# Performance work log

Hardware: AMD Instinct MI355X
Metric: run time of the kernel (lower is better)

The kernel has to match this reference:

```python
import jax, jax.numpy as jnp
import numpy as np

N, E, A, S = 100000, 1600000, 500000, 50000
F_IN, W, LAYERS = 64, 64, 3


def setup_inputs() -> dict:
    key = jax.random.key(0)
    ks = jax.random.split(key, 20)

    def glorot(k, shape):
        fan_in = shape[-2]
        return jax.random.normal(k, shape, dtype=jnp.float32) / jnp.sqrt(jnp.float32(fan_in))

    return {
        "x": jax.random.normal(ks[0], (N, F_IN), dtype=jnp.float32),
        "edge_src": jax.random.randint(ks[1], (E,), 0, N, dtype=jnp.int32),
        "edge_dst": jax.random.randint(ks[2], (E,), 0, N, dtype=jnp.int32),
        "gather_idx": jax.random.randint(ks[3], (A,), 0, N, dtype=jnp.int32),
        "seg_idx": jax.random.randint(ks[4], (A,), 0, S, dtype=jnp.int32),
        # GraphConv 0: lin_root (no bias) + lin_rel (bias)
        "w_root0": glorot(ks[5], (F_IN, W)),
        "w_rel0": glorot(ks[6], (F_IN, W)),
        "b0": jnp.zeros((W,), jnp.float32),
        # hidden GraphConv layers, stacked
        "w_root_h": glorot(ks[7], (LAYERS - 1, W, W)),
        "w_rel_h": glorot(ks[8], (LAYERS - 1, W, W)),
        "b_h": jnp.zeros((LAYERS - 1, W), jnp.float32),
        # MLP head
        "fc1_w": glorot(ks[9], (W, W)),
        "fc1_b": jnp.zeros((W,), jnp.float32),
        "fc2_w": glorot(ks[10], (W, 32)),
        "fc2_b": jnp.zeros((32,), jnp.float32),
        "fc3_w": glorot(ks[11], (32, 2)),
        "fc3_b": jnp.zeros((2,), jnp.float32),
        "num_sets": S,
    }


def _graph_conv(h, edge_src, edge_dst, w_root, w_rel, b):
    # PyG GraphConv (aggr='add'): out_i = W_root h_i + W_rel * sum_{j->i} h_j + b
    agg = jax.ops.segment_sum(h[edge_src], edge_dst, num_segments=h.shape[0])
    return h @ w_root + agg @ w_rel + b


def reference(x, edge_src, edge_dst, gather_idx, seg_idx,
              w_root0, w_rel0, b0, w_root_h, w_rel_h, b_h,
              fc1_w, fc1_b, fc2_w, fc2_b, fc3_w, fc3_b, num_sets):
    h = jax.nn.elu(_graph_conv(x, edge_src, edge_dst, w_root0, w_rel0, b0))
    for i in range(w_root_h.shape[0]):
        h = jax.nn.elu(_graph_conv(h, edge_src, edge_dst, w_root_h[i], w_rel_h[i], b_h[i]))
    # set pooling: gather node rows then scatter_add into sets
    pooled = jax.ops.segment_sum(h[gather_idx], seg_idx, num_segments=num_sets)  # [S, W]
    h = jax.nn.elu(pooled @ fc1_w + fc1_b)
    # dropout p=0.5 is identity at inference
    h = jax.nn.elu(h @ fc2_w + fc2_b)
    logits = h @ fc3_w + fc3_b
    return jax.nn.log_softmax(logits, axis=1)
```

## Files before the change

kernel.cpp:

```cpp
#include <hip/hip_runtime.h>


#define FEAT 64
#define SH 9
#define BSZ 512
#define CH 512
#define CAP 12288
#define SCHUNK 1024
#define IDXE 256
#define HPAD 8

typedef unsigned short u16;
typedef __attribute__((ext_vector_type(8))) short bf16x8;
typedef __attribute__((ext_vector_type(4))) float f32x4;

__device__ __forceinline__ float bf2f(u16 u) {
  union { unsigned int i; float f; } c; c.i = ((unsigned int)u) << 16; return c.f;
}
__device__ __forceinline__ u16 f2bf(float f) {
  union { float f; unsigned int i; } c; c.f = f;
  unsigned int u = c.i;
  return (u16)((u + 0x7FFFu + ((u >> 16) & 1u)) >> 16);
}

__global__ void p1a2_kernel(const int* __restrict__ k0, int* __restrict__ c0, int n0, int NB0,
                            const int* __restrict__ k1, int* __restrict__ c1, int n1, int NB1) {
  __shared__ int hist[256];
  int tid = threadIdx.x, b = blockIdx.x;
  const int* keys; int* counts; int nE, NB, c;
  if (b < CH) { keys = k0; counts = c0; nE = n0; NB = NB0; c = b; }
  else        { keys = k1; counts = c1; nE = n1; NB = NB1; c = b - CH; }
  hist[tid] = 0;
  __syncthreads();
  int len = (nE + CH - 1) / CH;
  int cbeg = c * len, cend = min(nE, cbeg + len);
  for (int i = cbeg + tid; i < cend; i += 256) atomicAdd(&hist[keys[i] >> SH], 1);
  __syncthreads();
  if (tid < NB) counts[tid * CH + c] = hist[tid];
}

__global__ void scan1_kernel(int* __restrict__ d0, int* __restrict__ bs0, int L0, int nb0,
                             int* __restrict__ d1, int* __restrict__ bs1, int L1) {
  __shared__ int tsum[256];
  int tid = threadIdx.x, b = blockIdx.x;
  int* data; int* bsums; int L, c;
  if (b < nb0) { data = d0; bsums = bs0; L = L0; c = b; }
  else         { data = d1; bsums = bs1; L = L1; c = b - nb0; }
  int base = c * SCHUNK + tid * 4;
  int v[4];
#pragma unroll
  for (int i = 0; i < 4; ++i) v[i] = (base + i < L) ? data[base + i] : 0;
  int local = v[0] + v[1] + v[2] + v[3];
  tsum[tid] = local;
  __syncthreads();
  for (int off = 1; off < 256; off <<= 1) {
    int u = (tid >= off) ? tsum[tid - off] : 0;
    __syncthreads();
    tsum[tid] += u;
    __syncthreads();
  }
  int excl = tsum[tid] - local;
  if (tid == 255) bsums[c] = tsum[255];
  int run = excl;
#pragma unroll
  for (int i = 0; i < 4; ++i) {
    if (base + i < L) data[base + i] = run;
    run += v[i];
  }
}

__global__ void scan2_kernel(int* __restrict__ bs0, int nb0, int* __restrict__ bs1, int nb1) {
  __shared__ int t[256];
  int tid = threadIdx.x;
  int* bsums = (blockIdx.x == 0) ? bs0 : bs1;
  int nb     = (blockIdx.x == 0) ? nb0 : nb1;
  int v = (tid < nb) ? bsums[tid] : 0;
  t[tid] = v;
  __syncthreads();
  for (int off = 1; off < 256; off <<= 1) {
    int u = (tid >= off) ? t[tid - off] : 0;
    __syncthreads();
    t[tid] += u;
    __syncthreads();
  }
  if (tid < nb) bsums[tid] = t[tid] - v;
}

__global__ void scan3_kernel(int* __restrict__ d0, const int* __restrict__ bs0,
                             int* __restrict__ bb0, int L0, int NB0, int tot0, int g0,
                             int* __restrict__ d1, const int* __restrict__ bs1,
                             int* __restrict__ bb1, int L1, int NB1, int tot1) {
  int b = blockIdx.x;
  int* data; const int* bsums; int* bbase; int L, NB, tot, i;
  if (b < g0) { data = d0; bsums = bs0; bbase = bb0; L = L0; NB = NB0; tot = tot0; i = b * 256 + threadIdx.x; }
  else        { data = d1; bsums = bs1; bbase = bb1; L = L1; NB = NB1; tot = tot1; i = (b - g0) * 256 + threadIdx.x; }
  if (i < L) {
    int v = data[i] + bsums[i / SCHUNK];
    data[i] = v;
    if ((i & (CH - 1)) == 0) bbase[i / CH] = v;
  }
  if (i == 0) bbase[NB] = tot;
}

__global__ void p1b2_kernel(const int* __restrict__ s0, const int* __restrict__ k0,
                            const int* __restrict__ c0, int* __restrict__ bin0, int n0, int NB0,
                            const int* __restrict__ s1, const int* __restrict__ k1,
                            const int* __restrict__ c1, int* __restrict__ bin1, int n1, int NB1) {
  __shared__ int cursor[256];
  int tid = threadIdx.x, b = blockIdx.x;
  const int* src; const int* keys; const int* counts; int* bin; int nE, NB, c;
  if (b < CH) { src = s0; keys = k0; counts = c0; bin = bin0; nE = n0; NB = NB0; c = b; }
  else        { src = s1; keys = k1; counts = c1; bin = bin1; nE = n1; NB = NB1; c = b - CH; }
  if (tid < NB) cursor[tid] = counts[tid * CH + c];
  __syncthreads();
  int len = (nE + CH - 1) / CH;
  int cbeg = c * len, cend = min(nE, cbeg + len);
  for (int i = cbeg + tid; i < cend; i += 256) {
    int k = keys[i];
    int bu = k >> SH;
    int pos = atomicAdd(&cursor[bu], 1);
    bin[pos] = (src[i] << SH) | (k & (BSZ - 1));
  }
}

__global__ void __launch_bounds__(256) p2_kernel(const int* __restrict__ bin0,
                                                 const int* __restrict__ bb0,
                                                 int* __restrict__ csr0, int* __restrict__ rs0,
                                                 int nn0, int NB0,
                                                 const int* __restrict__ bin1,
                                                 const int* __restrict__ bb1,
                                                 int* __restrict__ csr1, int* __restrict__ rs1,
                                                 int nn1) {
  __shared__ int s_csr[CAP];
  __shared__ int hist[BSZ];
  __shared__ int excl[BSZ];
  __shared__ int ts[256];
  int tid = threadIdx.x, bb = blockIdx.x;
  const int* bin; const int* bbase; int* csr; int* rs; int n_nodes, b;
  if (bb < NB0) { bin = bin0; bbase = bb0; csr = csr0; rs = rs0; n_nodes = nn0; b = bb; }
  else          { bin = bin1; bbase = bb1; csr = csr1; rs = rs1; n_nodes = nn1; b = bb - NB0; }
  int base = bbase[b];
  int cnt = bbase[b + 1] - base;
  int node_lo = b * BSZ;
  int nnode = min(BSZ, n_nodes - node_lo);

  hist[tid] = 0; hist[tid + 256] = 0;
  __syncthreads();
  for (int i = tid; i < cnt; i += 256) atomicAdd(&hist[bin[base + i] & (BSZ - 1)], 1);
  __syncthreads();

  int a0 = hist[2 * tid], a1 = hist[2 * tid + 1];
  int pair = a0 + a1;
  ts[tid] = pair;
  __syncthreads();
  for (int off = 1; off < 256; off <<= 1) {
    int u = (tid >= off) ? ts[tid - off] : 0;
    __syncthreads();
    ts[tid] += u;
    __syncthreads();
  }
  int pexcl = ts[tid] - pair;
  excl[2 * tid] = pexcl;
  excl[2 * tid + 1] = pexcl + a0;
  __syncthreads();

  for (int t = tid; t < nnode; t += 256) rs[node_lo + t] = base + excl[t];
  if (tid == 0 && node_lo + nnode >= n_nodes) rs[n_nodes] = bbase[(n_nodes + BSZ - 1) / BSZ];
  hist[tid] = excl[tid]; hist[tid + 256] = excl[tid + 256];
  __syncthreads();

  if (cnt <= CAP) {
    for (int i = tid; i < cnt; i += 256) {
      int e = bin[base + i];
      int pos = atomicAdd(&hist[e & (BSZ - 1)], 1);
      s_csr[pos] = e >> SH;
    }
    __syncthreads();
    for (int i = tid; i < cnt; i += 256) csr[base + i] = s_csr[i];
  } else {
    for (int i = tid; i < cnt; i += 256) {
      int e = bin[base + i];
      int pos = atomicAdd(&hist[e & (BSZ - 1)], 1);
      csr[base + pos] = e >> SH;
    }
  }
}

__global__ void cvt_bf16_kernel(const float* __restrict__ in, u16* __restrict__ out, int n4) {
  int i = blockIdx.x * 256 + threadIdx.x;
  if (i < n4) {
    float4 v = ((const float4*)in)[i];
    ushort4 o = { f2bf(v.x), f2bf(v.y), f2bf(v.z), f2bf(v.w) };
    ((ushort4*)out)[i] = o;
  }
}

__global__ void prepack_kernel(const float* __restrict__ w_root0, const float* __restrict__ w_rel0,
                               const float* __restrict__ w_root_h, const float* __restrict__ w_rel_h,
                               u16* __restrict__ wpack) {
  int l = blockIdx.x >> 4;
  int t = blockIdx.x & 15;
  int kt = t >> 2, nt = t & 3;
  int lane = threadIdx.x;
  const float* wr; const float* wl;
  if (l == 0) { wr = w_root0; wl = w_rel0; }
  else        { wr = w_root_h + (l - 1) * FEAT * FEAT; wl = w_rel_h + (l - 1) * FEAT * FEAT; }
  int n = nt * 16 + (lane & 15);
  int k0 = kt * 32 + (lane >> 4) * 8;
  u16* dst = wpack + (((size_t)l * 16 + t) * 64 + lane) * 8;
#pragma unroll
  for (int j = 0; j < 8; ++j) {
    int k = k0 + j;
    float v = (k < FEAT) ? wr[k * FEAT + n] : wl[(k - FEAT) * FEAT + n];
    dst[j] = f2bf(v);
  }
}

__device__ __forceinline__ float4 reduce_sub(float4 a) {
  a.x += __shfl_xor(a.x, 16, 64); a.y += __shfl_xor(a.y, 16, 64);
  a.z += __shfl_xor(a.z, 16, 64); a.w += __shfl_xor(a.w, 16, 64);
  a.x += __shfl_xor(a.x, 32, 64); a.y += __shfl_xor(a.y, 32, 64);
  a.z += __shfl_xor(a.z, 32, 64); a.w += __shfl_xor(a.w, 32, 64);
  return a;
}

__device__ __forceinline__ float4 wave_gather_acc(const u16* __restrict__ hb,
                                                  const int* idx,
                                                  int d, int sub, int ch) {
  float4 acc = {0.f, 0.f, 0.f, 0.f};
  int i = sub;
  for (; i + 12 < d; i += 16) {
    int s0 = idx[i];
    int s1 = idx[i + 4];
    int s2 = idx[i + 8];
    int s3 = idx[i + 12];
    ushort4 a = ((const ushort4*)(hb + (size_t)s0 * FEAT))[ch];
    ushort4 b = ((const ushort4*)(hb + (size_t)s1 * FEAT))[ch];
    ushort4 c = ((const ushort4*)(hb + (size_t)s2 * FEAT))[ch];
    ushort4 e = ((const ushort4*)(hb + (size_t)s3 * FEAT))[ch];
    acc.x += (bf2f(a.x) + bf2f(b.x)) + (bf2f(c.x) + bf2f(e.x));
    acc.y += (bf2f(a.y) + bf2f(b.y)) + (bf2f(c.y) + bf2f(e.y));
    acc.z += (bf2f(a.z) + bf2f(b.z)) + (bf2f(c.z) + bf2f(e.z));
    acc.w += (bf2f(a.w) + bf2f(b.w)) + (bf2f(c.w) + bf2f(e.w));
  }
  for (; i + 4 < d; i += 8) {
    int s0 = idx[i];
    int s1 = idx[i + 4];
    ushort4 a = ((const ushort4*)(hb + (size_t)s0 * FEAT))[ch];
    ushort4 b = ((const ushort4*)(hb + (size_t)s1 * FEAT))[ch];
    acc.x += bf2f(a.x) + bf2f(b.x);
    acc.y += bf2f(a.y) + bf2f(b.y);
    acc.z += bf2f(a.z) + bf2f(b.z);
    acc.w += bf2f(a.w) + bf2f(b.w);
  }
  if (i < d) {
    int s0 = idx[i];
    ushort4 a = ((const ushort4*)(hb + (size_t)s0 * FEAT))[ch];
    acc.x += bf2f(a.x); acc.y += bf2f(a.y);
    acc.z += bf2f(a.z); acc.w += bf2f(a.w);
  }
  return reduce_sub(acc);
}

__global__ void __launch_bounds__(512)
layer_fused_kernel(const u16* __restrict__ hb,
                   const int* __restrict__ rs,
                   const int* __restrict__ csr,
                   const u16* __restrict__ wpack,
                   const float* __restrict__ bias,
                   u16* __restrict__ outb, int n) {
  __shared__ u16 s_h[64][FEAT + HPAD];
  __shared__ u16 s_a[64][FEAT + HPAD];
  __shared__ int s_idx[8][IDXE];
  const int tid = threadIdx.x;
  const int wv = __builtin_amdgcn_readfirstlane(tid >> 6);
  const int lane = tid & 63;
  const int sub = lane >> 4;
  const int ch = lane & 15;
  const int base = blockIdx.x * 64;

  for (int it = 0; it < 2; ++it) {
    int idx = tid + it * 512;
    int nl = idx >> 4, c = idx & 15;
    int node = base + nl;
    if (node < n)
      *(ushort4*)&s_h[nl][c * 4] = ((const ushort4*)(hb + (size_t)node * FEAT))[c];
  }

  int wbase = base + wv * 8;
  if (wbase < n) {
    int r[9];
#pragma unroll
    for (int j = 0; j < 9; ++j) r[j] = rs[min(wbase + j, n)];
    int rbeg = r[0];
    int run = r[8] - rbeg;
    int* sidx = &s_idx[wv][0];
    bool staged = (run <= IDXE);
    if (staged) {
      for (int i = lane; i < run; i += 64) sidx[i] = csr[rbeg + i];
    }
    int nt = min(8, n - wbase);
    for (int t = 0; t < nt; ++t) {
      int dbeg = r[t] - rbeg;
      int d = r[t + 1] - r[t];
      float4 acc;
      if (staged) acc = wave_gather_acc(hb, sidx + dbeg, d, sub, ch);
      else        acc = wave_gather_acc(hb, csr + r[t], d, sub, ch);
      if (sub == 0) {
        ushort4 o = { f2bf(acc.x), f2bf(acc.y), f2bf(acc.z), f2bf(acc.w) };
        *(ushort4*)&s_a[wv * 8 + t][ch * 4] = o;
      }
    }
  }
  __syncthreads();

  const int mt = wv & 3;
  const int ntb = (wv >> 2) * 2;
  const int mrow = mt * 16 + (lane & 15);
  const int koff = (lane >> 4) * 8;
  f32x4 acc0 = {0.f, 0.f, 0.f, 0.f};
  f32x4 acc1 = {0.f, 0.f, 0.f, 0.f};
#pragma unroll
  for (int kt = 0; kt < 4; ++kt) {
    bf16x8 a;
    if (kt < 2) a = *(const bf16x8*)&s_h[mrow][kt * 32 + koff];
    else        a = *(const bf16x8*)&s_a[mrow][(kt - 2) * 32 + koff];
    bf16x8 b0 = *(const bf16x8*)&wpack[(((size_t)kt * 4 + ntb) * 64 + lane) * 8];
    bf16x8 b1 = *(const bf16x8*)&wpack[(((size_t)kt * 4 + ntb + 1) * 64 + lane) * 8];
    acc0 = __builtin_amdgcn_mfma_f32_16x16x32_bf16(a, b0, acc0, 0, 0, 0);
    acc1 = __builtin_amdgcn_mfma_f32_16x16x32_bf16(a, b1, acc1, 0, 0, 0);
  }
  __syncthreads();

  const int col = lane & 15;
  const int rbase = (lane >> 4) * 4;
  const float bs0 = bias[ntb * 16 + col];
  const float bs1 = bias[(ntb + 1) * 16 + col];
#pragma unroll
  for (int rg = 0; rg < 4; ++rg) {
    int nl = mt * 16 + rbase + rg;
    float v0 = acc0[rg] + bs0;
    float v1 = acc1[rg] + bs1;
    v0 = v0 > 0.f ? v0 : (__expf(v0) - 1.f);
    v1 = v1 > 0.f ? v1 : (__expf(v1) - 1.f);
    s_h[nl][ntb * 16 + col] = f2bf(v0);
    s_h[nl][(ntb + 1) * 16 + col] = f2bf(v1);
  }
  __syncthreads();

  for (int it = 0; it < 2; ++it) {
    int idx = tid + it * 512;
    int nl = idx >> 4, c = idx & 15;
    int node = base + nl;
    if (node < n)
      ((ushort4*)(outb + (size_t)node * FEAT))[c] = *(const ushort4*)&s_h[nl][c * 4];
  }
}

__global__ void __launch_bounds__(512)
pool_mlp_kernel(const u16* __restrict__ hb,
                const int* __restrict__ rs,
                const int* __restrict__ csr,
                const float* __restrict__ fc1_w, const float* __restrict__ fc1_b,
                const float* __restrict__ fc2_w, const float* __restrict__ fc2_b,
                const float* __restrict__ fc3_w, const float* __restrict__ fc3_b,
                float* __restrict__ out, int nsets) {
  __shared__ float s_p[64][FEAT + 4];
  __shared__ int s_idx[8][IDXE];
  const int tid = threadIdx.x;
  const int wv = __builtin_amdgcn_readfirstlane(tid >> 6);
  const int lane = tid & 63;
  const int sub = lane >> 4;
  const int ch = lane & 15;
  const int base = blockIdx.x * 64;

  int wbase = base + wv * 8;
  if (wbase < nsets) {
    int r[9];
#pragma unroll
    for (int j = 0; j < 9; ++j) r[j] = rs[min(wbase + j, nsets)];
    int rbeg = r[0];
    int run = r[8] - rbeg;
    int* sidx = &s_idx[wv][0];
    bool staged = (run <= IDXE);
    if (staged) {
      for (int i = lane; i < run; i += 64) sidx[i] = csr[rbeg + i];
    }
    int nt = min(8, nsets - wbase);
    for (int t = 0; t < nt; ++t) {
      int dbeg = r[t] - rbeg;
      int d = r[t + 1] - r[t];
      float4 acc;
      if (staged) acc = wave_gather_acc(hb, sidx + dbeg, d, sub, ch);
      else        acc = wave_gather_acc(hb, csr + r[t], d, sub, ch);
      if (sub == 0) *(float4*)&s_p[wv * 8 + t][ch * 4] = acc;
    }
  }
  __syncthreads();

  {
    const int jb = wv * 8;
    float acc[8];
#pragma unroll
    for (int jj = 0; jj < 8; ++jj) acc[jj] = fc1_b[jb + jj];
    for (int k = 0; k < FEAT; k += 4) {
      const float4 pv = *(const float4*)&s_p[lane][k];
      const float pk[4] = {pv.x, pv.y, pv.z, pv.w};
#pragma unroll
      for (int kk = 0; kk < 4; ++kk) {
        const float* w = fc1_w + (k + kk) * FEAT + jb;
#pragma unroll
        for (int jj = 0; jj < 8; ++jj) acc[jj] += pk[kk] * w[jj];
      }
    }
    __syncthreads();
#pragma unroll
    for (int jj = 0; jj < 8; ++jj) {
      float a = acc[jj];
      s_p[lane][jb + jj] = a > 0.f ? a : (__expf(a) - 1.f);
    }
  }
  __syncthreads();

  {
    const int jb = wv * 4;
    float acc[4];
#pragma unroll
    for (int jj = 0; jj < 4; ++jj) acc[jj] = fc2_b[jb + jj];
    for (int k = 0; k < FEAT; k += 4) {
      const float4 tv = *(const float4*)&s_p[lane][k];
      const float tk[4] = {tv.x, tv.y, tv.z, tv.w};
#pragma unroll
      for (int kk = 0; kk < 4; ++kk) {
        const float* w = fc2_w + (k + kk) * 32 + jb;
#pragma unroll
        for (int jj = 0; jj < 4; ++jj) acc[jj] += tk[kk] * w[jj];
      }
    }
    __syncthreads();
#pragma unroll
    for (int jj = 0; jj < 4; ++jj) {
      float a = acc[jj];
      s_p[lane][jb + jj] = a > 0.f ? a : (__expf(a) - 1.f);
    }
  }
  __syncthreads();

  if (wv == 0) {
    int s = base + lane;
    if (s < nsets) {
      float a0 = fc3_b[0], a1 = fc3_b[1];
      for (int k = 0; k < 32; k += 4) {
        const float4 tv = *(const float4*)&s_p[lane][k];
        const float tk[4] = {tv.x, tv.y, tv.z, tv.w};
#pragma unroll
        for (int kk = 0; kk < 4; ++kk) {
          a0 += tk[kk] * fc3_w[(k + kk) * 2 + 0];
          a1 += tk[kk] * fc3_w[(k + kk) * 2 + 1];
        }
      }
      float m = fmaxf(a0, a1);
      float lse = m + logf(__expf(a0 - m) + __expf(a1 - m));
      float2 r = {a0 - lse, a1 - lse};
      *(float2*)(out + (size_t)s * 2) = r;
    }
  }
}

extern "C" void kernel_launch(void* const* d_in, const int* in_sizes, int n_in,
                              void* d_out, int out_size, void* d_ws, size_t ws_size,
                              hipStream_t stream) {
  const float* x        = (const float*)d_in[0];
  const int* edge_src   = (const int*)d_in[1];
  const int* edge_dst   = (const int*)d_in[2];
  const int* gather_idx = (const int*)d_in[3];
  const int* seg_idx    = (const int*)d_in[4];
  const float* w_root0  = (const float*)d_in[5];
  const float* w_rel0   = (const float*)d_in[6];
  const float* b0       = (const float*)d_in[7];
  const float* w_root_h = (const float*)d_in[8];
  const float* w_rel_h  = (const float*)d_in[9];
  const float* b_h      = (const float*)d_in[10];
  const float* fc1_w    = (const float*)d_in[11];
  const float* fc1_b    = (const float*)d_in[12];
  const float* fc2_w    = (const float*)d_in[13];
  const float* fc2_b    = (const float*)d_in[14];
  const float* fc3_w    = (const float*)d_in[15];
  const float* fc3_b    = (const float*)d_in[16];

  const int N = in_sizes[0] / FEAT;
  const int E = in_sizes[1];
  const int A = in_sizes[3];
  const int S = out_size / 2;

  const int NB_e = (N + BSZ - 1) / BSZ;
  const int NB_p = (S + BSZ - 1) / BSZ;
  const int L_e = NB_e * CH, L_p = NB_p * CH;
  const int nb_e = (L_e + SCHUNK - 1) / SCHUNK;
  const int nb_p = (L_p + SCHUNK - 1) / SCHUNK;
  const int g_e = (L_e + 255) / 256, g_p = (L_p + 255) / 256;

  size_t hrow_bytes = (size_t)N * FEAT * sizeof(u16);
  char* ws = (char*)d_ws;
  size_t off = 0;
  auto alloc = [&](size_t bytes) { void* p = ws + off; off += (bytes + 15) & ~(size_t)15; return p; };
  u16* xb       = (u16*)alloc(hrow_bytes);
  u16* b1b      = (u16*)alloc(hrow_bytes);
  u16* b2b      = (u16*)alloc(hrow_bytes);
  int* csr_e    = (int*)alloc((size_t)E * 4);
  int* bin_e    = (int*)alloc((size_t)E * 4);
  int* rs_e     = (int*)alloc((size_t)(N + 1) * 4);
  int* counts_e = (int*)alloc((size_t)L_e * 4);
  int* bbase_e  = (int*)alloc((size_t)(NB_e + 1) * 4);
  int* csr_p    = (int*)alloc((size_t)A * 4);
  int* bin_p    = (int*)alloc((size_t)A * 4);
  int* rs_p     = (int*)alloc((size_t)(S + 1) * 4);
  int* counts_p = (int*)alloc((size_t)L_p * 4);
  int* bbase_p  = (int*)alloc((size_t)(NB_p + 1) * 4);
  int* bsums_e  = (int*)alloc(256 * 4);
  int* bsums_p  = (int*)alloc(256 * 4);
  u16* wpack    = (u16*)alloc((size_t)3 * 16 * 64 * 8 * sizeof(u16));

  dim3 blk(256);
  dim3 blk512(512);

  p1a2_kernel<<<2 * CH, blk, 0, stream>>>(edge_dst, counts_e, E, NB_e,
                                          seg_idx, counts_p, A, NB_p);
  scan1_kernel<<<nb_e + nb_p, blk, 0, stream>>>(counts_e, bsums_e, L_e, nb_e,
                                                counts_p, bsums_p, L_p);
  scan2_kernel<<<2, blk, 0, stream>>>(bsums_e, nb_e, bsums_p, nb_p);
  scan3_kernel<<<g_e + g_p, blk, 0, stream>>>(counts_e, bsums_e, bbase_e, L_e, NB_e, E, g_e,
                                              counts_p, bsums_p, bbase_p, L_p, NB_p, A);
  p1b2_kernel<<<2 * CH, blk, 0, stream>>>(edge_src, edge_dst, counts_e, bin_e, E, NB_e,
                                          gather_idx, seg_idx, counts_p, bin_p, A, NB_p);
  p2_kernel<<<NB_e + NB_p, blk, 0, stream>>>(bin_e, bbase_e, csr_e, rs_e, N, NB_e,
                                             bin_p, bbase_p, csr_p, rs_p, S);

  int n4 = N * FEAT / 4;
  cvt_bf16_kernel<<<(n4 + 255) / 256, blk, 0, stream>>>(x, xb, n4);
  prepack_kernel<<<48, dim3(64), 0, stream>>>(w_root0, w_rel0, w_root_h, w_rel_h, wpack);

  int lgrid = (N + 63) / 64;
  int pgrid = (S + 63) / 64;

  layer_fused_kernel<<<lgrid, blk512, 0, stream>>>(xb, rs_e, csr_e, wpack,
                                                   b0, b1b, N);
  layer_fused_kernel<<<lgrid, blk512, 0, stream>>>(b1b, rs_e, csr_e, wpack + 16 * 64 * 8,
                                                   b_h, b2b, N);
  layer_fused_kernel<<<lgrid, blk512, 0, stream>>>(b2b, rs_e, csr_e, wpack + 2 * 16 * 64 * 8,
                                                   b_h + FEAT, b1b, N);

  pool_mlp_kernel<<<pgrid, blk512, 0, stream>>>(b1b, rs_p, csr_p,
                                                fc1_w, fc1_b, fc2_w, fc2_b, fc3_w, fc3_b,
                                                (float*)d_out, S);
}
```

Baseline: 305.3 us.

## Replace multi-pass counting scan with atomic bucket totals and fuse preprocessing kernels

The per-chunk count matrix and its three-kernel scan are replaced by global atomic bucket totals, a single small scan, and per-chunk atomic cursor claims during the scatter. The bf16 conversion of the input and the weight prepacking are folded into the same launch as the histogram pass. The aim is fewer kernel launches and less intermediate memory traffic in the CSR-build preprocessing. In exchange the scatter kernel recomputes the local histogram, global atomics are added, and edge order within each bucket becomes nondeterministic.

After: 336.8 us. 10.3% more time.

```diff
diff --git a/kernel.cpp b/kernel.cpp
--- a/kernel.cpp
+++ b/kernel.cpp
@@ -6,7 +6,6 @@
 #define BSZ 512
 #define CH 512
 #define CAP 12288
-#define SCHUNK 1024
 #define IDXE 256
 #define HPAD 8
 
@@ -23,102 +22,100 @@
   return (u16)((u + 0x7FFFu + ((u >> 16) & 1u)) >> 16);
 }
 
-__global__ void p1a2_kernel(const int* __restrict__ k0, int* __restrict__ c0, int n0, int NB0,
-                            const int* __restrict__ k1, int* __restrict__ c1, int n1, int NB1) {
+__global__ void buildA_kernel(const int* __restrict__ kE, int* __restrict__ btotE, int nE, int NBe,
+                              const int* __restrict__ kP, int* __restrict__ btotP, int nP, int NBp,
+                              const float* __restrict__ x, u16* __restrict__ xb, int n4, int g_cvt,
+                              const float* __restrict__ wr0, const float* __restrict__ wl0,
+                              const float* __restrict__ wrh, const float* __restrict__ wlh,
+                              u16* __restrict__ wpack) {
   __shared__ int hist[256];
   int tid = threadIdx.x, b = blockIdx.x;
-  const int* keys; int* counts; int nE, NB, c;
-  if (b < CH) { keys = k0; counts = c0; nE = n0; NB = NB0; c = b; }
-  else        { keys = k1; counts = c1; nE = n1; NB = NB1; c = b - CH; }
+  if (b < 2 * CH) {
+    const int* keys; int* btot; int nK, NB, c;
+    if (b < CH) { keys = kE; btot = btotE; nK = nE; NB = NBe; c = b; }
+    else        { keys = kP; btot = btotP; nK = nP; NB = NBp; c = b - CH; }
+    hist[tid] = 0;
+    __syncthreads();
+    int len = (nK + CH - 1) / CH;
+    int cbeg = c * len, cend = min(nK, cbeg + len);
+    for (int i = cbeg + tid; i < cend; i += 256) atomicAdd(&hist[keys[i] >> SH], 1);
+    __syncthreads();
+    if (tid < NB && hist[tid] > 0) atomicAdd(&btot[tid], hist[tid]);
+  } else if (b < 2 * CH + g_cvt) {
+    int i = (b - 2 * CH) * 256 + tid;
+    if (i < n4) {
+      float4 v = ((const float4*)x)[i];
+      ushort4 o = { f2bf(v.x), f2bf(v.y), f2bf(v.z), f2bf(v.w) };
+      ((ushort4*)xb)[i] = o;
+    }
+  } else {
+    int t4 = (b - 2 * CH - g_cvt) * 4 + (tid >> 6);
+    if (t4 < 48) {
+      int l = t4 >> 4, t = t4 & 15;
+      int kt = t >> 2, nt = t & 3;
+      int lane = tid & 63;
+      const float* wr; const float* wl;
+      if (l == 0) { wr = wr0; wl = wl0; }
+      else        { wr = wrh + (l - 1) * FEAT * FEAT; wl = wlh + (l - 1) * FEAT * FEAT; }
+      int n = nt * 16 + (lane & 15);
+      int k0 = kt * 32 + (lane >> 4) * 8;
+      u16* dst = wpack + (((size_t)l * 16 + t) * 64 + lane) * 8;
+#pragma unroll
+      for (int j = 0; j < 8; ++j) {
+        int k = k0 + j;
+        float v = (k < FEAT) ? wr[k * FEAT + n] : wl[(k - FEAT) * FEAT + n];
+        dst[j] = f2bf(v);
+      }
+    }
+  }
+}
+
+__global__ void buildB_kernel(const int* __restrict__ btotE, int* __restrict__ bbE,
+                              int* __restrict__ curE, int NBe, int totE,
+                              const int* __restrict__ btotP, int* __restrict__ bbP,
+                              int* __restrict__ curP, int NBp, int totP) {
+  __shared__ int t[256];
+  int tid = threadIdx.x;
+  const int* btot; int* bb; int* cur; int NB, tot;
+  if (blockIdx.x == 0) { btot = btotE; bb = bbE; cur = curE; NB = NBe; tot = totE; }
+  else                 { btot = btotP; bb = bbP; cur = curP; NB = NBp; tot = totP; }
+  int v = (tid < NB) ? btot[tid] : 0;
+  t[tid] = v;
+  __syncthreads();
+  for (int off = 1; off < 256; off <<= 1) {
+    int u = (tid >= off) ? t[tid - off] : 0;
+    __syncthreads();
+    t[tid] += u;
+    __syncthreads();
+  }
+  int excl = t[tid] - v;
+  if (tid < NB) { bb[tid] = excl; cur[tid] = excl; }
+  if (tid == 0) bb[NB] = tot;
+}
+
+__global__ void buildC_kernel(const int* __restrict__ s0, const int* __restrict__ k0,
+                              int* __restrict__ cur0, int* __restrict__ bin0, int n0, int NB0,
+                              const int* __restrict__ s1, const int* __restrict__ k1,
+                              int* __restrict__ cur1, int* __restrict__ bin1, int n1, int NB1) {
+  __shared__ int hist[256];
+  int tid = threadIdx.x, b = blockIdx.x;
+  const int* src; const int* keys; int* cur; int* bin; int nE, NB, c;
+  if (b < CH) { src = s0; keys = k0; cur = cur0; bin = bin0; nE = n0; NB = NB0; c = b; }
+  else        { src = s1; keys = k1; cur = cur1; bin = bin1; nE = n1; NB = NB1; c = b - CH; }
   hist[tid] = 0;
   __syncthreads();
   int len = (nE + CH - 1) / CH;
   int cbeg = c * len, cend = min(nE, cbeg + len);
   for (int i = cbeg + tid; i < cend; i += 256) atomicAdd(&hist[keys[i] >> SH], 1);
   __syncthreads();
-  if (tid < NB) counts[tid * CH + c] = hist[tid];
-}
-
-__global__ void scan1_kernel(int* __restrict__ d0, int* __restrict__ bs0, int L0, int nb0,
-                             int* __restrict__ d1, int* __restrict__ bs1, int L1) {
-  __shared__ int tsum[256];
-  int tid = threadIdx.x, b = blockIdx.x;
-  int* data; int* bsums; int L, c;
-  if (b < nb0) { data = d0; bsums = bs0; L = L0; c = b; }
-  else         { data = d1; bsums = bs1; L = L1; c = b - nb0; }
-  int base = c * SCHUNK + tid * 4;
-  int v[4];
-#pragma unroll
-  for (int i = 0; i < 4; ++i) v[i] = (base + i < L) ? data[base + i] : 0;
-  int local = v[0] + v[1] + v[2] + v[3];
-  tsum[tid] = local;
-  __syncthreads();
-  for (int off = 1; off < 256; off <<= 1) {
-    int u = (tid >= off) ? tsum[tid - off] : 0;
-    __syncthreads();
-    tsum[tid] += u;
-    __syncthreads();
-  }
-  int excl = tsum[tid] - local;
-  if (tid == 255) bsums[c] = tsum[255];
-  int run = excl;
-#pragma unroll
-  for (int i = 0; i < 4; ++i) {
-    if (base + i < L) data[base + i] = run;
-    run += v[i];
-  }
-}
-
-__global__ void scan2_kernel(int* __restrict__ bs0, int nb0, int* __restrict__ bs1, int nb1) {
-  __shared__ int t[256];
-  int tid = threadIdx.x;
-  int* bsums = (blockIdx.x == 0) ? bs0 : bs1;
-  int nb     = (blockIdx.x == 0) ? nb0 : nb1;
-  int v = (tid < nb) ? bsums[tid] : 0;
-  t[tid] = v;
-  __syncthreads();
-  for (int off = 1; off < 256; off <<= 1) {
-    int u = (tid >= off) ? t[tid - off] : 0;
-    __syncthreads();
-    t[tid] += u;
-    __syncthreads();
-  }
-  if (tid < nb) bsums[tid] = t[tid] - v;
-}
-
-__global__ void scan3_kernel(int* __restrict__ d0, const int* __restrict__ bs0,
-                             int* __restrict__ bb0, int L0, int NB0, int tot0, int g0,
-                             int* __restrict__ d1, const int* __restrict__ bs1,
-                             int* __restrict__ bb1, int L1, int NB1, int tot1) {
-  int b = blockIdx.x;
-  int* data; const int* bsums; int* bbase; int L, NB, tot, i;
-  if (b < g0) { data = d0; bsums = bs0; bbase = bb0; L = L0; NB = NB0; tot = tot0; i = b * 256 + threadIdx.x; }
-  else        { data = d1; bsums = bs1; bbase = bb1; L = L1; NB = NB1; tot = tot1; i = (b - g0) * 256 + threadIdx.x; }
-  if (i < L) {
-    int v = data[i] + bsums[i / SCHUNK];
-    data[i] = v;
-    if ((i & (CH - 1)) == 0) bbase[i / CH] = v;
-  }
-  if (i == 0) bbase[NB] = tot;
-}
-
-__global__ void p1b2_kernel(const int* __restrict__ s0, const int* __restrict__ k0,
-                            const int* __restrict__ c0, int* __restrict__ bin0, int n0, int NB0,
-                            const int* __restrict__ s1, const int* __restrict__ k1,
-                            const int* __restrict__ c1, int* __restrict__ bin1, int n1, int NB1) {
-  __shared__ int cursor[256];
-  int tid = threadIdx.x, b = blockIdx.x;
-  const int* src; const int* keys; const int* counts; int* bin; int nE, NB, c;
-  if (b < CH) { src = s0; keys = k0; counts = c0; bin = bin0; nE = n0; NB = NB0; c = b; }
-  else        { src = s1; keys = k1; counts = c1; bin = bin1; nE = n1; NB = NB1; c = b - CH; }
-  if (tid < NB) cursor[tid] = counts[tid * CH + c];
-  __syncthreads();
-  int len = (nE + CH - 1) / CH;
-  int cbeg = c * len, cend = min(nE, cbeg + len);
+  int cnt = (tid < NB) ? hist[tid] : 0;
+  __syncthreads();
+  if (tid < NB) hist[tid] = (cnt > 0) ? atomicAdd(&cur[tid], cnt) : 0;
+  __syncthreads();
   for (int i = cbeg + tid; i < cend; i += 256) {
     int k = keys[i];
     int bu = k >> SH;
-    int pos = atomicAdd(&cursor[bu], 1);
+    int pos = atomicAdd(&hist[bu], 1);
     bin[pos] = (src[i] << SH) | (k & (BSZ - 1));
   }
 }
@@ -186,36 +183,6 @@
   }
 }
 
-__global__ void cvt_bf16_kernel(const float* __restrict__ in, u16* __restrict__ out, int n4) {
-  int i = blockIdx.x * 256 + threadIdx.x;
-  if (i < n4) {
-    float4 v = ((const float4*)in)[i];
-    ushort4 o = { f2bf(v.x), f2bf(v.y), f2bf(v.z), f2bf(v.w) };
-    ((ushort4*)out)[i] = o;
-  }
-}
-
-__global__ void prepack_kernel(const float* __restrict__ w_root0, const float* __restrict__ w_rel0,
-                               const float* __restrict__ w_root_h, const float* __restrict__ w_rel_h,
-                               u16* __restrict__ wpack) {
-  int l = blockIdx.x >> 4;
-  int t = blockIdx.x & 15;
-  int kt = t >> 2, nt = t & 3;
-  int lane = threadIdx.x;
-  const float* wr; const float* wl;
-  if (l == 0) { wr = w_root0; wl = w_rel0; }
-  else        { wr = w_root_h + (l - 1) * FEAT * FEAT; wl = w_rel_h + (l - 1) * FEAT * FEAT; }
-  int n = nt * 16 + (lane & 15);
-  int k0 = kt * 32 + (lane >> 4) * 8;
-  u16* dst = wpack + (((size_t)l * 16 + t) * 64 + lane) * 8;
-#pragma unroll
-  for (int j = 0; j < 8; ++j) {
-    int k = k0 + j;
-    float v = (k < FEAT) ? wr[k * FEAT + n] : wl[(k - FEAT) * FEAT + n];
-    dst[j] = f2bf(v);
-  }
-}
-
 __device__ __forceinline__ float4 reduce_sub(float4 a) {
   a.x += __shfl_xor(a.x, 16, 64); a.y += __shfl_xor(a.y, 16, 64);
   a.z += __shfl_xor(a.z, 16, 64); a.w += __shfl_xor(a.w, 16, 64);
@@ -230,10 +197,7 @@
   float4 acc = {0.f, 0.f, 0.f, 0.f};
   int i = sub;
   for (; i + 12 < d; i += 16) {
-    int s0 = idx[i];
-    int s1 = idx[i + 4];
-    int s2 = idx[i + 8];
-    int s3 = idx[i + 12];
+    int s0 = idx[i], s1 = idx[i + 4], s2 = idx[i + 8], s3 = idx[i + 12];
     ushort4 a = ((const ushort4*)(hb + (size_t)s0 * FEAT))[ch];
     ushort4 b = ((const ushort4*)(hb + (size_t)s1 * FEAT))[ch];
     ushort4 c = ((const ushort4*)(hb + (size_t)s2 * FEAT))[ch];
@@ -244,8 +208,7 @@
     acc.w += (bf2f(a.w) + bf2f(b.w)) + (bf2f(c.w) + bf2f(e.w));
   }
   for (; i + 4 < d; i += 8) {
-    int s0 = idx[i];
-    int s1 = idx[i + 4];
+    int s0 = idx[i], s1 = idx[i + 4];
     ushort4 a = ((const ushort4*)(hb + (size_t)s0 * FEAT))[ch];
     ushort4 b = ((const ushort4*)(hb + (size_t)s1 * FEAT))[ch];
     acc.x += bf2f(a.x) + bf2f(b.x);
@@ -301,10 +264,9 @@
     }
     int nt = min(8, n - wbase);
     for (int t = 0; t < nt; ++t) {
-      int dbeg = r[t] - rbeg;
       int d = r[t + 1] - r[t];
       float4 acc;
-      if (staged) acc = wave_gather_acc(hb, sidx + dbeg, d, sub, ch);
+      if (staged) acc = wave_gather_acc(hb, sidx + (r[t] - rbeg), d, sub, ch);
       else        acc = wave_gather_acc(hb, csr + r[t], d, sub, ch);
       if (sub == 0) {
         ushort4 o = { f2bf(acc.x), f2bf(acc.y), f2bf(acc.z), f2bf(acc.w) };
@@ -388,10 +350,9 @@
     }
     int nt = min(8, nsets - wbase);
     for (int t = 0; t < nt; ++t) {
-      int dbeg = r[t] - rbeg;
       int d = r[t + 1] - r[t];
       float4 acc;
-      if (staged) acc = wave_gather_acc(hb, sidx + dbeg, d, sub, ch);
+      if (staged) acc = wave_gather_acc(hb, sidx + (r[t] - rbeg), d, sub, ch);
       else        acc = wave_gather_acc(hb, csr + r[t], d, sub, ch);
       if (sub == 0) *(float4*)&s_p[wv * 8 + t][ch * 4] = acc;
     }
@@ -495,10 +456,6 @@
 
   const int NB_e = (N + BSZ - 1) / BSZ;
   const int NB_p = (S + BSZ - 1) / BSZ;
-  const int L_e = NB_e * CH, L_p = NB_p * CH;
-  const int nb_e = (L_e + SCHUNK - 1) / SCHUNK;
-  const int nb_p = (L_p + SCHUNK - 1) / SCHUNK;
-  const int g_e = (L_e + 255) / 256, g_p = (L_p + 255) / 256;
 
   size_t hrow_bytes = (size_t)N * FEAT * sizeof(u16);
   char* ws = (char*)d_ws;
@@ -510,35 +467,34 @@
   int* csr_e    = (int*)alloc((size_t)E * 4);
   int* bin_e    = (int*)alloc((size_t)E * 4);
   int* rs_e     = (int*)alloc((size_t)(N + 1) * 4);
-  int* counts_e = (int*)alloc((size_t)L_e * 4);
-  int* bbase_e  = (int*)alloc((size_t)(NB_e + 1) * 4);
   int* csr_p    = (int*)alloc((size_t)A * 4);
   int* bin_p    = (int*)alloc((size_t)A * 4);
   int* rs_p     = (int*)alloc((size_t)(S + 1) * 4);
-  int* counts_p = (int*)alloc((size_t)L_p * 4);
+  int* btot_e   = (int*)alloc((size_t)(NB_e) * 4);
+  int* btot_p   = (int*)alloc((size_t)(NB_p) * 4);
+  int* bbase_e  = (int*)alloc((size_t)(NB_e + 1) * 4);
   int* bbase_p  = (int*)alloc((size_t)(NB_p + 1) * 4);
-  int* bsums_e  = (int*)alloc(256 * 4);
-  int* bsums_p  = (int*)alloc(256 * 4);
+  int* cur_e    = (int*)alloc((size_t)NB_e * 4);
+  int* cur_p    = (int*)alloc((size_t)NB_p * 4);
   u16* wpack    = (u16*)alloc((size_t)3 * 16 * 64 * 8 * sizeof(u16));
 
   dim3 blk(256);
   dim3 blk512(512);
 
-  p1a2_kernel<<<2 * CH, blk, 0, stream>>>(edge_dst, counts_e, E, NB_e,
-                                          seg_idx, counts_p, A, NB_p);
-  scan1_kernel<<<nb_e + nb_p, blk, 0, stream>>>(counts_e, bsums_e, L_e, nb_e,
-                                                counts_p, bsums_p, L_p);
-  scan2_kernel<<<2, blk, 0, stream>>>(bsums_e, nb_e, bsums_p, nb_p);
-  scan3_kernel<<<g_e + g_p, blk, 0, stream>>>(counts_e, bsums_e, bbase_e, L_e, NB_e, E, g_e,
-                                              counts_p, bsums_p, bbase_p, L_p, NB_p, A);
-  p1b2_kernel<<<2 * CH, blk, 0, stream>>>(edge_src, edge_dst, counts_e, bin_e, E, NB_e,
-                                          gather_idx, seg_idx, counts_p, bin_p, A, NB_p);
+  int n4 = N * FEAT / 4;
+  int g_cvt = (n4 + 255) / 256;
+  int g_pp = 12;
+
+  hipMemsetAsync(btot_e, 0, (size_t)(NB_e + NB_p) * 4 + 16, stream);
+  buildA_kernel<<<2 * CH + g_cvt + g_pp, blk, 0, stream>>>(
+      edge_dst, btot_e, E, NB_e, seg_idx, btot_p, A, NB_p,
+      x, xb, n4, g_cvt, w_root0, w_rel0, w_root_h, w_rel_h, wpack);
+  buildB_kernel<<<2, blk, 0, stream>>>(btot_e, bbase_e, cur_e, NB_e, E,
+                                       btot_p, bbase_p, cur_p, NB_p, A);
+  buildC_kernel<<<2 * CH, blk, 0, stream>>>(edge_src, edge_dst, cur_e, bin_e, E, NB_e,
+                                            gather_idx, seg_idx, cur_p, bin_p, A, NB_p);
   p2_kernel<<<NB_e + NB_p, blk, 0, stream>>>(bin_e, bbase_e, csr_e, rs_e, N, NB_e,
                                              bin_p, bbase_p, csr_p, rs_p, S);
-
-  int n4 = N * FEAT / 4;
-  cvt_bf16_kernel<<<(n4 + 255) / 256, blk, 0, stream>>>(x, xb, n4);
-  prepack_kernel<<<48, dim3(64), 0, stream>>>(w_root0, w_rel0, w_root_h, w_rel_h, wpack);
 
   int lgrid = (N + 63) / 64;
   int pgrid = (S + 63) / 64;
```

## Fuse bf16 convert and weight prepack into histogram kernel; stage binning scatter in LDS

Applied to the files above, without the earlier changes.

Folds the input bf16 conversion and the weight prepack into the first histogram kernel as extra blocks, removing two launches. It also rewrites the bin-scatter pass to compute a block-local prefix over buckets and sort each chunk in shared memory first. Each chunk is then written to the global bins as contiguous runs instead of scattered atomic-positioned stores. This adds a second key pass, an LDS scan with extra barriers, and shared-memory use that may lower occupancy.

New measurement: 301.4 us (median of 2 runs). No clear change (-1.3%).

```diff
diff --git a/kernel.cpp b/kernel.cpp
--- a/kernel.cpp
+++ b/kernel.cpp
@@ -9,6 +9,7 @@
 #define SCHUNK 1024
 #define IDXE 256
 #define HPAD 8
+#define LCHUNK 3200
 
 typedef unsigned short u16;
 typedef __attribute__((ext_vector_type(8))) short bf16x8;
@@ -23,20 +24,52 @@
   return (u16)((u + 0x7FFFu + ((u >> 16) & 1u)) >> 16);
 }
 
-__global__ void p1a2_kernel(const int* __restrict__ k0, int* __restrict__ c0, int n0, int NB0,
-                            const int* __restrict__ k1, int* __restrict__ c1, int n1, int NB1) {
+__global__ void p1a2f_kernel(const int* __restrict__ kE, int* __restrict__ cE, int nE, int NBe,
+                             const int* __restrict__ kP, int* __restrict__ cP, int nP, int NBp,
+                             const float* __restrict__ x, u16* __restrict__ xb, int n4, int g_cvt,
+                             const float* __restrict__ wr0, const float* __restrict__ wl0,
+                             const float* __restrict__ wrh, const float* __restrict__ wlh,
+                             u16* __restrict__ wpack) {
   __shared__ int hist[256];
   int tid = threadIdx.x, b = blockIdx.x;
-  const int* keys; int* counts; int nE, NB, c;
-  if (b < CH) { keys = k0; counts = c0; nE = n0; NB = NB0; c = b; }
-  else        { keys = k1; counts = c1; nE = n1; NB = NB1; c = b - CH; }
-  hist[tid] = 0;
-  __syncthreads();
-  int len = (nE + CH - 1) / CH;
-  int cbeg = c * len, cend = min(nE, cbeg + len);
-  for (int i = cbeg + tid; i < cend; i += 256) atomicAdd(&hist[keys[i] >> SH], 1);
-  __syncthreads();
-  if (tid < NB) counts[tid * CH + c] = hist[tid];
+  if (b < 2 * CH) {
+    const int* keys; int* counts; int nK, NB, c;
+    if (b < CH) { keys = kE; counts = cE; nK = nE; NB = NBe; c = b; }
+    else        { keys = kP; counts = cP; nK = nP; NB = NBp; c = b - CH; }
+    hist[tid] = 0;
+    __syncthreads();
+    int len = (nK + CH - 1) / CH;
+    int cbeg = c * len, cend = min(nK, cbeg + len);
+    for (int i = cbeg + tid; i < cend; i += 256) atomicAdd(&hist[keys[i] >> SH], 1);
+    __syncthreads();
+    if (tid < NB) counts[tid * CH + c] = hist[tid];
+  } else if (b < 2 * CH + g_cvt) {
+    int i = (b - 2 * CH) * 256 + tid;
+    if (i < n4) {
+      float4 v = ((const float4*)x)[i];
+      ushort4 o = { f2bf(v.x), f2bf(v.y), f2bf(v.z), f2bf(v.w) };
+      ((ushort4*)xb)[i] = o;
+    }
+  } else {
+    int t4 = (b - 2 * CH - g_cvt) * 4 + (tid >> 6);
+    if (t4 < 48) {
+      int l = t4 >> 4, t = t4 & 15;
+      int kt = t >> 2, nt = t & 3;
+      int lane = tid & 63;
+      const float* wr; const float* wl;
+      if (l == 0) { wr = wr0; wl = wl0; }
+      else        { wr = wrh + (l - 1) * FEAT * FEAT; wl = wlh + (l - 1) * FEAT * FEAT; }
+      int n = nt * 16 + (lane & 15);
+      int k0 = kt * 32 + (lane >> 4) * 8;
+      u16* dst = wpack + (((size_t)l * 16 + t) * 64 + lane) * 8;
+#pragma unroll
+      for (int j = 0; j < 8; ++j) {
+        int k = k0 + j;
+        float v = (k < FEAT) ? wr[k * FEAT + n] : wl[(k - FEAT) * FEAT + n];
+        dst[j] = f2bf(v);
+      }
+    }
+  }
 }
 
 __global__ void scan1_kernel(int* __restrict__ d0, int* __restrict__ bs0, int L0, int nb0,
@@ -102,24 +135,64 @@
   if (i == 0) bbase[NB] = tot;
 }
 
-__global__ void p1b2_kernel(const int* __restrict__ s0, const int* __restrict__ k0,
-                            const int* __restrict__ c0, int* __restrict__ bin0, int n0, int NB0,
-                            const int* __restrict__ s1, const int* __restrict__ k1,
-                            const int* __restrict__ c1, int* __restrict__ bin1, int n1, int NB1) {
-  __shared__ int cursor[256];
+__global__ void __launch_bounds__(256)
+p1b2_kernel(const int* __restrict__ s0, const int* __restrict__ k0,
+            const int* __restrict__ c0, int* __restrict__ bin0, int n0, int NB0,
+            const int* __restrict__ s1, const int* __restrict__ k1,
+            const int* __restrict__ c1, int* __restrict__ bin1, int n1, int NB1) {
+  __shared__ int s_bin[LCHUNK];
+  __shared__ unsigned char s_bu[LCHUNK];
+  __shared__ int lcur[256];
+  __shared__ int gdiff[256];
+  __shared__ int ts[256];
   int tid = threadIdx.x, b = blockIdx.x;
   const int* src; const int* keys; const int* counts; int* bin; int nE, NB, c;
   if (b < CH) { src = s0; keys = k0; counts = c0; bin = bin0; nE = n0; NB = NB0; c = b; }
   else        { src = s1; keys = k1; counts = c1; bin = bin1; nE = n1; NB = NB1; c = b - CH; }
-  if (tid < NB) cursor[tid] = counts[tid * CH + c];
-  __syncthreads();
   int len = (nE + CH - 1) / CH;
   int cbeg = c * len, cend = min(nE, cbeg + len);
-  for (int i = cbeg + tid; i < cend; i += 256) {
-    int k = keys[i];
-    int bu = k >> SH;
-    int pos = atomicAdd(&cursor[bu], 1);
-    bin[pos] = (src[i] << SH) | (k & (BSZ - 1));
+  int L = cend - cbeg;
+
+  lcur[tid] = 0;
+  __syncthreads();
+  for (int i = cbeg + tid; i < cend; i += 256) atomicAdd(&lcur[keys[i] >> SH], 1);
+  __syncthreads();
+
+  int v = lcur[tid];
+  ts[tid] = v;
+  __syncthreads();
+  for (int off = 1; off < 256; off <<= 1) {
+    int u = (tid >= off) ? ts[tid - off] : 0;
+    __syncthreads();
+    ts[tid] += u;
+    __syncthreads();
+  }
+  int excl = ts[tid] - v;
+  __syncthreads();
+  lcur[tid] = excl;
+  gdiff[tid] = ((tid < NB) ? counts[tid * CH + c] : 0) - excl;
+  __syncthreads();
+
+  if (L <= LCHUNK) {
+    for (int i = cbeg + tid; i < cend; i += 256) {
+      int k = keys[i];
+      int bu = k >> SH;
+      int pos = atomicAdd(&lcur[bu], 1);
+      s_bin[pos] = (src[i] << SH) | (k & (BSZ - 1));
+      s_bu[pos] = (unsigned char)bu;
+    }
+    __syncthreads();
+    for (int i = tid; i < L; i += 256) {
+      int bu = s_bu[i];
+      bin[gdiff[bu] + i] = s_bin[i];
+    }
+  } else {
+    for (int i = cbeg + tid; i < cend; i += 256) {
+      int k = keys[i];
+      int bu = k >> SH;
+      int pos = atomicAdd(&lcur[bu], 1);
+      bin[gdiff[bu] + pos] = (src[i] << SH) | (k & (BSZ - 1));
+    }
   }
 }
 
@@ -186,36 +259,6 @@
   }
 }
 
-__global__ void cvt_bf16_kernel(const float* __restrict__ in, u16* __restrict__ out, int n4) {
-  int i = blockIdx.x * 256 + threadIdx.x;
-  if (i < n4) {
-    float4 v = ((const float4*)in)[i];
-    ushort4 o = { f2bf(v.x), f2bf(v.y), f2bf(v.z), f2bf(v.w) };
-    ((ushort4*)out)[i] = o;
-  }
-}
-
-__global__ void prepack_kernel(const float* __restrict__ w_root0, const float* __restrict__ w_rel0,
-                               const float* __restrict__ w_root_h, const float* __restrict__ w_rel_h,
-                               u16* __restrict__ wpack) {
-  int l = blockIdx.x >> 4;
-  int t = blockIdx.x & 15;
-  int kt = t >> 2, nt = t & 3;
-  int lane = threadIdx.x;
-  const float* wr; const float* wl;
-  if (l == 0) { wr = w_root0; wl = w_rel0; }
-  else        { wr = w_root_h + (l - 1) * FEAT * FEAT; wl = w_rel_h + (l - 1) * FEAT * FEAT; }
-  int n = nt * 16 + (lane & 15);
-  int k0 = kt * 32 + (lane >> 4) * 8;
-  u16* dst = wpack + (((size_t)l * 16 + t) * 64 + lane) * 8;
-#pragma unroll
-  for (int j = 0; j < 8; ++j) {
-    int k = k0 + j;
-    float v = (k < FEAT) ? wr[k * FEAT + n] : wl[(k - FEAT) * FEAT + n];
-    dst[j] = f2bf(v);
-  }
-}
-
 __device__ __forceinline__ float4 reduce_sub(float4 a) {
   a.x += __shfl_xor(a.x, 16, 64); a.y += __shfl_xor(a.y, 16, 64);
   a.z += __shfl_xor(a.z, 16, 64); a.w += __shfl_xor(a.w, 16, 64);
@@ -230,10 +273,7 @@
   float4 acc = {0.f, 0.f, 0.f, 0.f};
   int i = sub;
   for (; i + 12 < d; i += 16) {
-    int s0 = idx[i];
-    int s1 = idx[i + 4];
-    int s2 = idx[i + 8];
-    int s3 = idx[i + 12];
+    int s0 = idx[i], s1 = idx[i + 4], s2 = idx[i + 8], s3 = idx[i + 12];
     ushort4 a = ((const ushort4*)(hb + (size_t)s0 * FEAT))[ch];
     ushort4 b = ((const ushort4*)(hb + (size_t)s1 * FEAT))[ch];
     ushort4 c = ((const ushort4*)(hb + (size_t)s2 * FEAT))[ch];
@@ -244,8 +284,7 @@
     acc.w += (bf2f(a.w) + bf2f(b.w)) + (bf2f(c.w) + bf2f(e.w));
   }
   for (; i + 4 < d; i += 8) {
-    int s0 = idx[i];
-    int s1 = idx[i + 4];
+    int s0 = idx[i], s1 = idx[i + 4];
     ushort4 a = ((const ushort4*)(hb + (size_t)s0 * FEAT))[ch];
     ushort4 b = ((const ushort4*)(hb + (size_t)s1 * FEAT))[ch];
     acc.x += bf2f(a.x) + bf2f(b.x);
@@ -301,10 +340,9 @@
     }
     int nt = min(8, n - wbase);
     for (int t = 0; t < nt; ++t) {
-      int dbeg = r[t] - rbeg;
       int d = r[t + 1] - r[t];
       float4 acc;
-      if (staged) acc = wave_gather_acc(hb, sidx + dbeg, d, sub, ch);
+      if (staged) acc = wave_gather_acc(hb, sidx + (r[t] - rbeg), d, sub, ch);
       else        acc = wave_gather_acc(hb, csr + r[t], d, sub, ch);
       if (sub == 0) {
         ushort4 o = { f2bf(acc.x), f2bf(acc.y), f2bf(acc.z), f2bf(acc.w) };
@@ -388,10 +426,9 @@
     }
     int nt = min(8, nsets - wbase);
     for (int t = 0; t < nt; ++t) {
-      int dbeg = r[t] - rbeg;
       int d = r[t + 1] - r[t];
       float4 acc;
-      if (staged) acc = wave_gather_acc(hb, sidx + dbeg, d, sub, ch);
+      if (staged) acc = wave_gather_acc(hb, sidx + (r[t] - rbeg), d, sub, ch);
       else        acc = wave_gather_acc(hb, csr + r[t], d, sub, ch);
       if (sub == 0) *(float4*)&s_p[wv * 8 + t][ch * 4] = acc;
     }
@@ -524,8 +561,13 @@
   dim3 blk(256);
   dim3 blk512(512);
 
-  p1a2_kernel<<<2 * CH, blk, 0, stream>>>(edge_dst, counts_e, E, NB_e,
-                                          seg_idx, counts_p, A, NB_p);
+  int n4 = N * FEAT / 4;
+  int g_cvt = (n4 + 255) / 256;
+  int g_pp = 12;
+
+  p1a2f_kernel<<<2 * CH + g_cvt + g_pp, blk, 0, stream>>>(
+      edge_dst, counts_e, E, NB_e, seg_idx, counts_p, A, NB_p,
+      x, xb, n4, g_cvt, w_root0, w_rel0, w_root_h, w_rel_h, wpack);
   scan1_kernel<<<nb_e + nb_p, blk, 0, stream>>>(counts_e, bsums_e, L_e, nb_e,
                                                 counts_p, bsums_p, L_p);
   scan2_kernel<<<2, blk, 0, stream>>>(bsums_e, nb_e, bsums_p, nb_p);
@@ -536,10 +578,6 @@
   p2_kernel<<<NB_e + NB_p, blk, 0, stream>>>(bin_e, bbase_e, csr_e, rs_e, N, NB_e,
                                              bin_p, bbase_p, csr_p, rs_p, S);
 
-  int n4 = N * FEAT / 4;
-  cvt_bf16_kernel<<<(n4 + 255) / 256, blk, 0, stream>>>(x, xb, n4);
-  prepack_kernel<<<48, dim3(64), 0, stream>>>(w_root0, w_rel0, w_root_h, w_rel_h, wpack);
-
   int lgrid = (N + 63) / 64;
   int pgrid = (S + 63) / 64;
 
```
